# Kernel optimization log

Hardware: AMD Instinct MI355X
Metric: run time of the kernel (lower is better)

Reference implementation:

```python
import jax, jax.numpy as jnp
import numpy as np

B, N, K, H, W = 8, 16, 128, 64, 64
POS_RATE = 0.002  # fraction of positive heatmap pixels


def setup_inputs() -> dict:
    key = jax.random.key(0)
    k1, k2, k3 = jax.random.split(key, 3)
    # scores in (0.01, 0.99) so log(s) and log(1-s) are finite
    all_scores = jax.random.uniform(k1, (B, K, N), dtype=jnp.float32) * 0.98 + 0.01
    gt_heatmap = (jax.random.uniform(k2, (B, N, H, W)) < POS_RATE).astype(jnp.float32)
    # guarantee at least one positive pixel per heatmap (original errors on empty nonzero)
    gt_heatmap = gt_heatmap.at[:, :, 0, 0].set(1.0)
    keypoints_list = jax.random.uniform(k3, (B, K, 2), dtype=jnp.float32) * H
    return {"all_scores": all_scores, "gt_heatmap": gt_heatmap, "keypoints_list": keypoints_list}


def reference(all_scores, gt_heatmap, keypoints_list):
    Bs, Ns, Hs, Ws = gt_heatmap.shape
    # pixel coordinates in (row, col) order, matching torch nonzero() output
    hh, ww = jnp.meshgrid(jnp.arange(Hs, dtype=jnp.float32),
                          jnp.arange(Ws, dtype=jnp.float32), indexing='ij')
    coords = jnp.stack([hh.ravel(), ww.ravel()], axis=-1)  # [HW, 2]

    # distance from every candidate keypoint to every pixel: [B, K, HW]
    diff = keypoints_list[:, :, None, :] - coords[None, None, :, :]
    dist = jnp.sqrt(jnp.sum(diff * diff, axis=-1))

    mask = gt_heatmap.reshape(Bs, Ns, -1) > 0  # [B, N, HW]
    # min distance to any ground-truth pixel of heatmap n: [B, N, K]
    dmin = jnp.min(jnp.where(mask[:, :, None, :], dist[:, None, :, :], jnp.inf), axis=-1)

    scores = jnp.transpose(all_scores, (0, 2, 1))  # [B, N, K]
    pos = dmin < 1.0
    dsafe = jnp.where(pos, dmin, 0.0)  # avoid inf/overflow in unused branch
    pos_loss = jnp.sum(jnp.where(pos, 10000.0 / (1.0 + jnp.exp(dsafe)) * jnp.log(scores), 0.0))
    neg_loss = jnp.sum(jnp.where(pos, 0.0, jnp.log(1.0 - scores)))
    neg_count = jnp.sum(~pos)

    loss = -pos_loss - jnp.where(neg_count > 0,
                                 10000.0 / neg_count.astype(jnp.float32) * neg_loss,
                                 0.0)
    return loss
```

## Files before the change

### kernel.cpp

```cpp
#include <hip/hip_runtime.h>

#define BB 8
#define NN 16
#define KK 128
#define HH 64
#define WW 64
#define HWPX (HH * WW)
#define NBLK (BB * NN)

#define WS_P0 0
#define WS_P1 NBLK
#define WS_P2 (2 * NBLK)
#define WS_CNT_BYTE_OFF (3 * NBLK * sizeof(float))

__global__ __launch_bounds__(128) void kp_loss_fused(
    const float* __restrict__ all_scores,
    const float* __restrict__ gt_heatmap,
    const float* __restrict__ keypoints,
    float* __restrict__ ws,
    unsigned int* __restrict__ done_cnt,
    float* __restrict__ out)
{
    __shared__ float sh_r[HWPX];
    __shared__ float sh_c[HWPX];
    __shared__ int   sh_count;
    __shared__ float wred[2][3];
    __shared__ int   sh_last;

    const int blk  = blockIdx.x;
    const int b    = blk >> 4;
    const int n    = blk & (NN - 1);
    const int tid  = threadIdx.x;
    const int lane = tid & 63;
    const int wid  = tid >> 6;

    if (tid == 0) sh_count = 0;
    __syncthreads();

    const float4* hm = (const float4*)(gt_heatmap + (size_t)blk * HWPX);
    for (int i = tid; i < HWPX / 4; i += 128) {
        const float4 v = hm[i];
        const int base = i << 2;
        const float row = (float)(base >> 6);
        const float col = (float)(base & (WW - 1));
        if (v.x > 0.0f) { int s = atomicAdd(&sh_count, 1); sh_r[s] = row; sh_c[s] = col; }
        if (v.y > 0.0f) { int s = atomicAdd(&sh_count, 1); sh_r[s] = row; sh_c[s] = col + 1.0f; }
        if (v.z > 0.0f) { int s = atomicAdd(&sh_count, 1); sh_r[s] = row; sh_c[s] = col + 2.0f; }
        if (v.w > 0.0f) { int s = atomicAdd(&sh_count, 1); sh_r[s] = row; sh_c[s] = col + 3.0f; }
    }
    __syncthreads();
    const int cnt = sh_count;

    const float kr = keypoints[((size_t)b * KK + tid) * 2 + 0];
    const float kc = keypoints[((size_t)b * KK + tid) * 2 + 1];
    float dmin2 = INFINITY;
    for (int m = 0; m < cnt; ++m) {
        const float dr = kr - sh_r[m];
        const float dc = kc - sh_c[m];
        dmin2 = fminf(dmin2, dr * dr + dc * dc);
    }
    const float score = all_scores[((size_t)b * KK + tid) * NN + n];
    float r0 = 0.0f, r1 = 0.0f, r2 = 0.0f;
    if (dmin2 < 1.0f) {
        r0 = 10000.0f / (1.0f + __expf(sqrtf(dmin2))) * __logf(score);
    } else {
        r1 = __logf(1.0f - score);
        r2 = 1.0f;
    }

    for (int off = 32; off > 0; off >>= 1) {
        r0 += __shfl_down(r0, off);
        r1 += __shfl_down(r1, off);
        r2 += __shfl_down(r2, off);
    }
    if (lane == 0) { wred[wid][0] = r0; wred[wid][1] = r1; wred[wid][2] = r2; }
    __syncthreads();

    if (tid == 0) {
        __hip_atomic_store(&ws[WS_P0 + blk], wred[0][0] + wred[1][0],
                           __ATOMIC_RELAXED, __HIP_MEMORY_SCOPE_AGENT);
        __hip_atomic_store(&ws[WS_P1 + blk], wred[0][1] + wred[1][1],
                           __ATOMIC_RELAXED, __HIP_MEMORY_SCOPE_AGENT);
        __hip_atomic_store(&ws[WS_P2 + blk], wred[0][2] + wred[1][2],
                           __ATOMIC_RELAXED, __HIP_MEMORY_SCOPE_AGENT);
        const unsigned int old = __hip_atomic_fetch_add(done_cnt, 1u, __ATOMIC_ACQ_REL,
                                                        __HIP_MEMORY_SCOPE_AGENT);
        sh_last = ((old & (NBLK - 1)) == NBLK - 1);
    }
    __syncthreads();

    if (sh_last) {
        float p0 = __hip_atomic_load(&ws[WS_P0 + tid], __ATOMIC_RELAXED, __HIP_MEMORY_SCOPE_AGENT);
        float p1 = __hip_atomic_load(&ws[WS_P1 + tid], __ATOMIC_RELAXED, __HIP_MEMORY_SCOPE_AGENT);
        float p2 = __hip_atomic_load(&ws[WS_P2 + tid], __ATOMIC_RELAXED, __HIP_MEMORY_SCOPE_AGENT);
        for (int off = 32; off > 0; off >>= 1) {
            p0 += __shfl_down(p0, off);
            p1 += __shfl_down(p1, off);
            p2 += __shfl_down(p2, off);
        }
        if (lane == 0) { wred[wid][0] = p0; wred[wid][1] = p1; wred[wid][2] = p2; }
        __syncthreads();
        if (tid == 0) {
            const float pos_sum = wred[0][0] + wred[1][0];
            const float neg_sum = wred[0][1] + wred[1][1];
            const float cntf    = wred[0][2] + wred[1][2];
            float loss = -pos_sum;
            if (cntf > 0.0f) loss -= (10000.0f / cntf) * neg_sum;
            out[0] = loss;
        }
    }
}

extern "C" void kernel_launch(void* const* d_in, const int* in_sizes, int n_in,
                              void* d_out, int out_size, void* d_ws, size_t ws_size,
                              hipStream_t stream) {
    const float* all_scores = (const float*)d_in[0];
    const float* gt_heatmap = (const float*)d_in[1];
    const float* keypoints  = (const float*)d_in[2];
    float* out = (float*)d_out;
    float* ws  = (float*)d_ws;
    unsigned int* done_cnt = (unsigned int*)((char*)d_ws + WS_CNT_BYTE_OFF);

    kp_loss_fused<<<NBLK, 128, 0, stream>>>(all_scores, gt_heatmap, keypoints,
                                            ws, done_cnt, out);
}
```

Baseline: 11.41 us.

## Replace full heatmap scan with 4-corner neighborhood lookup per keypoint

Since only distances below 1 affect the loss, each keypoint now checks just the four integer pixels surrounding it instead of compacting all positive pixels of the heatmap into shared memory and scanning them. This removes the full 16 KB-per-block heatmap read, the shared atomics and the O(count) distance loop, replacing them with scattered 4-element gathers. Atomic orders for the cross-block partial sums are also strengthened to release/acquire.

```diff
diff --git a/kernel.cpp b/kernel.cpp
--- a/kernel.cpp
+++ b/kernel.cpp
@@ -13,7 +13,7 @@
 #define WS_P2 (2 * NBLK)
 #define WS_CNT_BYTE_OFF (3 * NBLK * sizeof(float))
 
-__global__ __launch_bounds__(128) void kp_loss_fused(
+__global__ __launch_bounds__(128) void kp_loss_corner(
     const float* __restrict__ all_scores,
     const float* __restrict__ gt_heatmap,
     const float* __restrict__ keypoints,
@@ -21,9 +21,6 @@
     unsigned int* __restrict__ done_cnt,
     float* __restrict__ out)
 {
-    __shared__ float sh_r[HWPX];
-    __shared__ float sh_c[HWPX];
-    __shared__ int   sh_count;
     __shared__ float wred[2][3];
     __shared__ int   sh_last;
 
@@ -34,55 +31,55 @@
     const int lane = tid & 63;
     const int wid  = tid >> 6;
 
-    if (tid == 0) sh_count = 0;
-    __syncthreads();
-
-    const float4* hm = (const float4*)(gt_heatmap + (size_t)blk * HWPX);
-    for (int i = tid; i < HWPX / 4; i += 128) {
-        const float4 v = hm[i];
-        const int base = i << 2;
-        const float row = (float)(base >> 6);
-        const float col = (float)(base & (WW - 1));
-        if (v.x > 0.0f) { int s = atomicAdd(&sh_count, 1); sh_r[s] = row; sh_c[s] = col; }
-        if (v.y > 0.0f) { int s = atomicAdd(&sh_count, 1); sh_r[s] = row; sh_c[s] = col + 1.0f; }
-        if (v.z > 0.0f) { int s = atomicAdd(&sh_count, 1); sh_r[s] = row; sh_c[s] = col + 2.0f; }
-        if (v.w > 0.0f) { int s = atomicAdd(&sh_count, 1); sh_r[s] = row; sh_c[s] = col + 3.0f; }
-    }
-    __syncthreads();
-    const int cnt = sh_count;
-
     const float kr = keypoints[((size_t)b * KK + tid) * 2 + 0];
     const float kc = keypoints[((size_t)b * KK + tid) * 2 + 1];
+    const float* hm = gt_heatmap + (size_t)blk * HWPX;
+
+    const int r0 = (int)floorf(kr);
+    const int c0 = (int)floorf(kc);
+
     float dmin2 = INFINITY;
-    for (int m = 0; m < cnt; ++m) {
-        const float dr = kr - sh_r[m];
-        const float dc = kc - sh_c[m];
-        dmin2 = fminf(dmin2, dr * dr + dc * dc);
+    #pragma unroll
+    for (int ri = 0; ri < 2; ++ri) {
+        #pragma unroll
+        for (int ci = 0; ci < 2; ++ci) {
+            const int r = r0 + ri;
+            const int c = c0 + ci;
+            if (r < HH && c < WW) {
+                if (hm[r * WW + c] > 0.0f) {
+                    const float dr = __fsub_rn(kr, (float)r);
+                    const float dc = __fsub_rn(kc, (float)c);
+                    const float d2 = __fadd_rn(__fmul_rn(dr, dr), __fmul_rn(dc, dc));
+                    dmin2 = fminf(dmin2, d2);
+                }
+            }
+        }
     }
+
     const float score = all_scores[((size_t)b * KK + tid) * NN + n];
-    float r0 = 0.0f, r1 = 0.0f, r2 = 0.0f;
+    float r0v = 0.0f, r1v = 0.0f, r2v = 0.0f;
     if (dmin2 < 1.0f) {
-        r0 = 10000.0f / (1.0f + __expf(sqrtf(dmin2))) * __logf(score);
+        r0v = 10000.0f / (1.0f + __expf(__fsqrt_rn(dmin2))) * __logf(score);
     } else {
-        r1 = __logf(1.0f - score);
-        r2 = 1.0f;
+        r1v = __logf(1.0f - score);
+        r2v = 1.0f;
     }
 
     for (int off = 32; off > 0; off >>= 1) {
-        r0 += __shfl_down(r0, off);
-        r1 += __shfl_down(r1, off);
-        r2 += __shfl_down(r2, off);
+        r0v += __shfl_down(r0v, off);
+        r1v += __shfl_down(r1v, off);
+        r2v += __shfl_down(r2v, off);
     }
-    if (lane == 0) { wred[wid][0] = r0; wred[wid][1] = r1; wred[wid][2] = r2; }
+    if (lane == 0) { wred[wid][0] = r0v; wred[wid][1] = r1v; wred[wid][2] = r2v; }
     __syncthreads();
 
     if (tid == 0) {
         __hip_atomic_store(&ws[WS_P0 + blk], wred[0][0] + wred[1][0],
-                           __ATOMIC_RELAXED, __HIP_MEMORY_SCOPE_AGENT);
+                           __ATOMIC_RELEASE, __HIP_MEMORY_SCOPE_AGENT);
         __hip_atomic_store(&ws[WS_P1 + blk], wred[0][1] + wred[1][1],
-                           __ATOMIC_RELAXED, __HIP_MEMORY_SCOPE_AGENT);
+                           __ATOMIC_RELEASE, __HIP_MEMORY_SCOPE_AGENT);
         __hip_atomic_store(&ws[WS_P2 + blk], wred[0][2] + wred[1][2],
-                           __ATOMIC_RELAXED, __HIP_MEMORY_SCOPE_AGENT);
+                           __ATOMIC_RELEASE, __HIP_MEMORY_SCOPE_AGENT);
         const unsigned int old = __hip_atomic_fetch_add(done_cnt, 1u, __ATOMIC_ACQ_REL,
                                                         __HIP_MEMORY_SCOPE_AGENT);
         sh_last = ((old & (NBLK - 1)) == NBLK - 1);
@@ -90,9 +87,9 @@
     __syncthreads();
 
     if (sh_last) {
-        float p0 = __hip_atomic_load(&ws[WS_P0 + tid], __ATOMIC_RELAXED, __HIP_MEMORY_SCOPE_AGENT);
-        float p1 = __hip_atomic_load(&ws[WS_P1 + tid], __ATOMIC_RELAXED, __HIP_MEMORY_SCOPE_AGENT);
-        float p2 = __hip_atomic_load(&ws[WS_P2 + tid], __ATOMIC_RELAXED, __HIP_MEMORY_SCOPE_AGENT);
+        float p0 = __hip_atomic_load(&ws[WS_P0 + tid], __ATOMIC_ACQUIRE, __HIP_MEMORY_SCOPE_AGENT);
+        float p1 = __hip_atomic_load(&ws[WS_P1 + tid], __ATOMIC_ACQUIRE, __HIP_MEMORY_SCOPE_AGENT);
+        float p2 = __hip_atomic_load(&ws[WS_P2 + tid], __ATOMIC_ACQUIRE, __HIP_MEMORY_SCOPE_AGENT);
         for (int off = 32; off > 0; off >>= 1) {
             p0 += __shfl_down(p0, off);
             p1 += __shfl_down(p1, off);
@@ -121,6 +118,6 @@
     float* ws  = (float*)d_ws;
     unsigned int* done_cnt = (unsigned int*)((char*)d_ws + WS_CNT_BYTE_OFF);
 
-    kp_loss_fused<<<NBLK, 128, 0, stream>>>(all_scores, gt_heatmap, keypoints,
-                                            ws, done_cnt, out);
+    kp_loss_corner<<<NBLK, 128, 0, stream>>>(all_scores, gt_heatmap, keypoints,
+                                             ws, done_cnt, out);
 }
```

Result: slower. 13.83 us (+21.2%).
